# Kernel tuning notes

Hardware: AMD Instinct MI355X
Metric: run time of the kernel (lower is better)

## Reference

```python
import jax, jax.numpy as jnp
import numpy as np

B, C, H, W = 8, 256, 64, 64
K = 64  # tfam_channels

def _conv3x3(x, w, b):
    # x: [B,C,H,W], w: [O,I,3,3]
    y = jax.lax.conv_general_dilated(x, w, window_strides=(1, 1), padding='SAME',
                                     dimension_numbers=('NCHW', 'OIHW', 'NCHW'))
    return y + b[None, :, None, None]

def setup_inputs() -> dict:
    key = jax.random.key(0)
    ks = jax.random.split(key, 5)
    s1 = 1.0 / np.sqrt(C)
    s3 = 1.0 / np.sqrt(C * 9)
    return {
        'x': jax.random.normal(ks[0], (B, C, H, W), jnp.float32),
        'top_w': jax.random.normal(ks[1], (K, C), jnp.float32) * s1,
        'top_b': jnp.zeros((K,), jnp.float32),
        'center_w': jax.random.normal(ks[2], (K, C), jnp.float32) * s1,
        'center_b': jnp.zeros((K,), jnp.float32),
        'bottom_w': jax.random.normal(ks[3], (C, C, 3, 3), jnp.float32) * s3,
        'bottom_b': jnp.zeros((C,), jnp.float32),
        'out_w': jax.random.normal(ks[4], (C, C, 3, 3), jnp.float32) * s3,
        'out_b': jnp.zeros((C,), jnp.float32),
    }

def reference(x, top_w, top_b, center_w, center_b, bottom_w, bottom_b, out_w, out_b):
    b, c, h, w = x.shape
    hw = h * w
    # 1x1 convs as channel contractions
    x_top = jnp.einsum('bchw,kc->bkhw', x, top_w) + top_b[None, :, None, None]
    x_center = jnp.einsum('bchw,kc->bkhw', x, center_w) + center_b[None, :, None, None]
    x_bottom = _conv3x3(x, bottom_w, bottom_b)

    x_top = x_top.reshape(b, -1, hw)                     # [B,K,HW]
    x_center = x_center.reshape(b, -1, hw)               # [B,K,HW]
    x_bot = x_bottom.reshape(b, c, hw).transpose(0, 2, 1)  # [B,HW,C]

    sp_map = jnp.einsum('bkn,bkm->bnm', x_center, x_top)  # [B,HW,HW]
    # global softmax over the entire flattened map per batch element
    sp_map = jax.nn.softmax(sp_map.reshape(b, -1), axis=1).reshape(b, hw, hw)
    sp_map = jnp.einsum('bnm,bmc->bnc', sp_map, x_bot)    # [B,HW,C]
    # faithful raw reshape (as in the torch code: no transpose)
    sp_map = sp_map.reshape(b, c, h, w)
    y = x + sp_map
    return _conv3x3(y, out_w, out_b)
```

## Files before the change

### kernel.cpp

```cpp
#include <hip/hip_runtime.h>

using bf16x8 = __attribute__((ext_vector_type(8))) short;
using f16x8  = __attribute__((ext_vector_type(8))) _Float16;
using f32x4  = __attribute__((ext_vector_type(4))) float;

#define DEVI static __device__ __forceinline__

DEVI unsigned short f2bf(float f){
  unsigned u = __builtin_bit_cast(unsigned, f);
  u += 0x7fffu + ((u >> 16) & 1u);
  return (unsigned short)(u >> 16);
}
DEVI unsigned short f2h(float f){
  _Float16 h = (_Float16)f;
  return __builtin_bit_cast(unsigned short, h);
}
DEVI f32x4 zf4(){ f32x4 z; z[0]=0.f; z[1]=0.f; z[2]=0.f; z[3]=0.f; return z; }

__global__ __launch_bounds__(256) void k_prep(
    const float* __restrict__ top_w, const float* __restrict__ cen_w,
    const float* __restrict__ bot_w, const float* __restrict__ out_w,
    float* __restrict__ wTt, float* __restrict__ wTc,
    unsigned short* __restrict__ apb, unsigned short* __restrict__ apo){
  int i = blockIdx.x * 256 + threadIdx.x;
  if (i < 64 * 256){
    int c = i >> 6, k = i & 63;
    wTt[i] = top_w[k * 256 + c];
    wTc[i] = cen_w[k * 256 + c];
  }
  if (i < 9 * 256 * 256){
    int tau = i >> 16, oc = i & 65535;
    apb[i] = f2bf(bot_w[oc * 9 + tau]);
    apo[i] = f2bf(out_w[oc * 9 + tau]);
  }
}

__global__ __launch_bounds__(256) void k_topcenter(
    const float* __restrict__ x,
    const float* __restrict__ wTt, const float* __restrict__ wTc,
    const float* __restrict__ top_b, const float* __restrict__ cen_b,
    unsigned short* __restrict__ tT16, unsigned short* __restrict__ cT16){
  __shared__ float xs[16][256];
  int b = blockIdx.z, z = blockIdx.y, nt = blockIdx.x;
  int t = threadIdx.x;
  int n = nt * 256 + t;
  const float* wT   = z ? wTc : wTt;
  const float* bias = z ? cen_b : top_b;
  unsigned short* o16 = z ? cT16 : tT16;
  const float scale = z ? 1.0f : 1.4426950408889634f;
  const float* xb = x + ((size_t)b << 20);

  float acc[64];
  #pragma unroll
  for (int k = 0; k < 64; k++) acc[k] = 0.f;

  for (int cc = 0; cc < 256; cc += 16){
    __syncthreads();
    #pragma unroll
    for (int r = 0; r < 16; r++)
      xs[r][t] = xb[((size_t)(cc + r) << 12) + nt * 256 + t];
    __syncthreads();
    #pragma unroll
    for (int r = 0; r < 16; r++){
      float xv = xs[r][t];
      const float* wr = wT + (cc + r) * 64;
      #pragma unroll
      for (int k = 0; k < 64; k++) acc[k] = fmaf(wr[k], xv, acc[k]);
    }
  }
  size_t base = (((size_t)b << 12) + n) * 64;
  #pragma unroll
  for (int k8 = 0; k8 < 64; k8 += 8){
    bf16x8 v8;
    #pragma unroll
    for (int j = 0; j < 8; j++)
      v8[j] = (short)f2h((acc[k8 + j] + bias[k8 + j]) * scale);
    *(bf16x8*)(o16 + base + k8) = v8;
  }
}

__global__ __launch_bounds__(256) void k_trans(
    const float* __restrict__ x, const float* __restrict__ U0,
    const float* __restrict__ U1, const float* __restrict__ Z,
    unsigned short* __restrict__ ocl){
  __shared__ float tile[32][33];
  int b = blockIdx.z, ct = blockIdx.y, pt = blockIdx.x;
  int tx = threadIdx.x & 31, ty = threadIdx.x >> 5;
  size_t bo = (size_t)b << 20;
  int c0 = ct * 32, p0 = pt * 32;
  float invZ = (U0 != nullptr) ? (1.0f / Z[b]) : 0.0f;
  #pragma unroll
  for (int q = 0; q < 4; q++){
    int c = c0 + ty + q * 8;
    size_t idx = bo + ((size_t)c << 12) + p0 + tx;
    float v = x[idx];
    if (U0){
      float u = U0[idx];
      if (U1) u += U1[idx];
      v = fmaf(u, invZ, v);
    }
    tile[ty + q * 8][tx] = v;
  }
  __syncthreads();
  #pragma unroll
  for (int q = 0; q < 4; q++){
    int p = p0 + ty + q * 8;
    ocl[bo + ((size_t)p << 8) + c0 + tx] = f2bf(tile[tx][ty + q * 8]);
  }
}

template<int OUTF32>
__global__ __launch_bounds__(256, 4) void k_conv3(
    const unsigned short* __restrict__ incl,
    const unsigned short* __restrict__ ap,
    const float* __restrict__ bias, void* __restrict__ outp){
  __shared__ unsigned short Xs[3][64][72];
  int bid = blockIdx.x;
  int b = bid & 7, h = (bid >> 3) & 63, oh = bid >> 9;
  int t = threadIdx.x, wv = t >> 6, l = t & 63, lr = l & 15, g = l >> 4;
  int o0 = oh * 128 + wv * 32;
  const unsigned short* inb = incl + ((size_t)b << 20);

  f32x4 acc[2][4];
  #pragma unroll
  for (int a = 0; a < 2; a++)
    #pragma unroll
    for (int c = 0; c < 4; c++) acc[a][c] = zf4();

  int sw = t >> 2, sco = (t & 3) * 16;
  const bf16x8 zero8 = {0,0,0,0,0,0,0,0};

  bf16x8 st[3][2];
  #pragma unroll
  for (int r = 0; r < 3; r++){
    int h2 = h + r - 1;
    bool v = (unsigned)h2 < 64u;
    #pragma unroll
    for (int u = 0; u < 2; u++)
      st[r][u] = v ? *(const bf16x8*)(inb + (((size_t)(h2 * 64 + sw)) << 8)
                                      + sco + u * 8)
                   : zero8;
  }

  for (int cc = 0; cc < 256; cc += 64){
    __syncthreads();
    #pragma unroll
    for (int r = 0; r < 3; r++)
      #pragma unroll
      for (int u = 0; u < 2; u++)
        *(bf16x8*)(&Xs[r][sw][sco + u * 8]) = st[r][u];
    __syncthreads();
    if (cc < 192){
      #pragma unroll
      for (int r = 0; r < 3; r++){
        int h2 = h + r - 1;
        bool v = (unsigned)h2 < 64u;
        #pragma unroll
        for (int u = 0; u < 2; u++)
          st[r][u] = v ? *(const bf16x8*)(inb + (((size_t)(h2 * 64 + sw)) << 8)
                                          + cc + 64 + sco + u * 8)
                       : zero8;
      }
    }
    #pragma unroll
    for (int tau = 0; tau < 9; tau++){
      int dy = tau / 3 - 1, dx = tau % 3 - 1;
      #pragma unroll
      for (int kf = 0; kf < 2; kf++){
        bf16x8 af[2];
        #pragma unroll
        for (int of = 0; of < 2; of++)
          af[of] = *(const bf16x8*)(ap + ((size_t)tau << 16)
                     + ((o0 + of * 16 + lr) << 8) + cc + kf * 32 + 8 * g);
        bf16x8 bv[4];
        #pragma unroll
        for (int pf = 0; pf < 4; pf++){
          int wsrc = pf * 16 + lr + dx;
          bv[pf] = ((unsigned)wsrc < 64u)
                 ? *(const bf16x8*)(&Xs[dy + 1][wsrc][kf * 32 + 8 * g])
                 : zero8;
        }
        #pragma unroll
        for (int of = 0; of < 2; of++)
          #pragma unroll
          for (int pf = 0; pf < 4; pf++)
            acc[of][pf] = __builtin_amdgcn_mfma_f32_16x16x32_bf16(af[of], bv[pf], acc[of][pf], 0, 0, 0);
      }
    }
  }
  #pragma unroll
  for (int of = 0; of < 2; of++){
    int ob = o0 + of * 16 + 4 * g;
    #pragma unroll
    for (int pf = 0; pf < 4; pf++){
      int p = h * 64 + pf * 16 + lr;
      #pragma unroll
      for (int i = 0; i < 4; i++){
        int o = ob + i;
        float v = acc[of][pf][i] + bias[o];
        size_t oi = ((size_t)b << 20) + ((size_t)o << 12) + p;
        if (OUTF32) ((float*)outp)[oi] = v;
        else        ((unsigned short*)outp)[oi] = f2bf(v);
      }
    }
  }
}

__global__ __launch_bounds__(256, 2) void k_pv(
    const unsigned short* __restrict__ tT16, const unsigned short* __restrict__ cT16,
    const unsigned short* __restrict__ xbot,
    float* __restrict__ U0, float* __restrict__ U1,
    float* __restrict__ rsum, int nsteps){
  __shared__ unsigned short Pl[2][64 * 64];
  __shared__ unsigned short Xl[2][256 * 64];
  int bid = blockIdx.x;
  int b = bid & 7, nt = (bid >> 3) & 63, mh = bid >> 9;
  int t = threadIdx.x, wv = t >> 6, l = t & 63, lr = l & 15, g = l >> 4;
  int n0 = nt * 64;
  const unsigned short* xbb = xbot + ((size_t)b << 20);
  float* Ub = mh ? U1 : U0;

  f16x8 ch[2][4];
  #pragma unroll
  for (int kf = 0; kf < 2; kf++)
    #pragma unroll
    for (int nf = 0; nf < 4; nf++)
      ch[kf][nf] = *(const f16x8*)(cT16
          + (((size_t)b << 12) + n0 + nf * 16 + lr) * 64 + kf * 32 + 8 * g);

  f32x4 acc[4][4];
  #pragma unroll
  for (int a = 0; a < 4; a++)
    #pragma unroll
    for (int c = 0; c < 4; c++) acc[a][c] = zf4();
  float racc = 0.f;
  unsigned pk[4][2];

  int srow = wv * 8 + (l >> 3);
  const unsigned short* gstage = xbb + ((size_t)srow << 12) + (size_t)mh * 2048
      + (((l & 7) ^ ((l >> 3) & 7)) << 3);

  const unsigned short* tb = tT16
      + (((size_t)b << 12) + (size_t)mh * 2048 + wv * 16 + lr) * 64 + 8 * g;

  auto gll = [&](int buf, int step){
    const unsigned short* gs = gstage + (size_t)step * 64;
    #pragma unroll
    for (int j = 0; j < 8; j++)
      __builtin_amdgcn_global_load_lds(
          (const __attribute__((address_space(1))) void*)(gs + ((size_t)(32 * j) << 12)),
          (__attribute__((address_space(3))) void*)(&Xl[buf][(wv * 8 + j * 32) * 64]),
          16, 0, 0);
  };

  auto sphase = [&](f16x8 A0, f16x8 A1){
    f32x4 sa[4];
    #pragma unroll
    for (int nf = 0; nf < 4; nf++) sa[nf] = zf4();
    #pragma unroll
    for (int nf = 0; nf < 4; nf++)
      sa[nf] = __builtin_amdgcn_mfma_f32_16x16x32_f16(A0, ch[0][nf], sa[nf], 0, 0, 0);
    #pragma unroll
    for (int nf = 0; nf < 4; nf++)
      sa[nf] = __builtin_amdgcn_mfma_f32_16x16x32_f16(A1, ch[1][nf], sa[nf], 0, 0, 0);
    #pragma unroll
    for (int nf = 0; nf < 4; nf++){
      float e0 = __builtin_amdgcn_exp2f(sa[nf][0]);
      float e1 = __builtin_amdgcn_exp2f(sa[nf][1]);
      float e2 = __builtin_amdgcn_exp2f(sa[nf][2]);
      float e3 = __builtin_amdgcn_exp2f(sa[nf][3]);
      racc += (e0 + e1) + (e2 + e3);
      pk[nf][0] = (unsigned)f2bf(e0) | ((unsigned)f2bf(e1) << 16);
      pk[nf][1] = (unsigned)f2bf(e2) | ((unsigned)f2bf(e3) << 16);
    }
  };

  auto plwrite = [&](int buf){
    #pragma unroll
    for (int nf = 0; nf < 4; nf++){
      unsigned* pp = (unsigned*)(&Pl[buf][(nf * 16 + lr) * 64
          + (((2 * wv + (g >> 1)) ^ (lr & 7)) << 3) + ((g & 1) << 2)]);
      pp[0] = pk[nf][0];
      pp[1] = pk[nf][1];
    }
  };

  auto pv = [&](int buf){
    #pragma unroll
    for (int kf = 0; kf < 2; kf++){
      bf16x8 pa[4];
      #pragma unroll
      for (int nf = 0; nf < 4; nf++)
        pa[nf] = *(const bf16x8*)(&Pl[buf][(nf * 16 + lr) * 64
                   + ((((kf << 2) + g) ^ (lr & 7)) << 3)]);
      #pragma unroll
      for (int cf = 0; cf < 4; cf++){
        bf16x8 bx = *(const bf16x8*)(&Xl[buf][(wv * 64 + cf * 16 + lr) * 64
                   + ((((kf << 2) + g) ^ (lr & 7)) << 3)]);
        #pragma unroll
        for (int nf = 0; nf < 4; nf++)
          acc[nf][cf] = __builtin_amdgcn_mfma_f32_16x16x32_bf16(pa[nf], bx, acc[nf][cf], 0, 0, 0);
      }
    }
  };

  f16x8 a0 = *(const f16x8*)(tb);
  f16x8 a1 = *(const f16x8*)(tb + 32);
  gll(0, 0);
  sphase(a0, a1);
  a0 = *(const f16x8*)(tb + (size_t)4096);
  a1 = *(const f16x8*)(tb + (size_t)4096 + 32);
  plwrite(0);
  __syncthreads();

  for (int ms = 0; ms < nsteps; ms++){
    int cur = ms & 1, nxt = cur ^ 1;
    if (ms + 1 < nsteps){
      gll(nxt, ms + 1);
      sphase(a0, a1);
      if (ms + 2 < nsteps){
        a0 = *(const f16x8*)(tb + (size_t)(ms + 2) * 4096);
        a1 = *(const f16x8*)(tb + (size_t)(ms + 2) * 4096 + 32);
      }
    }
    pv(cur);
    if (ms + 1 < nsteps) plwrite(nxt);
    __syncthreads();
  }

  #pragma unroll
  for (int nf = 0; nf < 4; nf++)
    #pragma unroll
    for (int cf = 0; cf < 4; cf++)
      #pragma unroll
      for (int i = 0; i < 4; i++){
        int n = n0 + nf * 16 + 4 * g + i;
        int c = wv * 64 + cf * 16 + lr;
        __builtin_nontemporal_store(acc[nf][cf][i],
            &Ub[((size_t)b << 20) + ((size_t)n << 8) + c]);
      }
  racc += __shfl_xor(racc, 1);
  racc += __shfl_xor(racc, 2);
  racc += __shfl_xor(racc, 4);
  racc += __shfl_xor(racc, 8);
  racc += __shfl_xor(racc, 16);
  racc += __shfl_xor(racc, 32);
  if (l == 0) rsum[(size_t)bid * 4 + wv] = racc;
}

__global__ __launch_bounds__(256) void k_rsum(const float* __restrict__ r,
                                              float* __restrict__ Z, int msplit){
  __shared__ float red[256];
  int b = blockIdx.x, t = threadIdx.x;
  int total = 256 * msplit;
  float s = 0.f;
  for (int s2 = t; s2 < total; s2 += 256)
    s += r[(size_t)(b + 8 * (s2 >> 2)) * 4 + (s2 & 3)];
  red[t] = s;
  __syncthreads();
  for (int o = 128; o > 0; o >>= 1){
    if (t < o) red[t] += red[t + o];
    __syncthreads();
  }
  if (t == 0) Z[b] = red[0];
}

extern "C" void kernel_launch(void* const* d_in, const int* in_sizes, int n_in,
                              void* d_out, int out_size, void* d_ws, size_t ws_size,
                              hipStream_t stream) {
  const float* x     = (const float*)d_in[0];
  const float* top_w = (const float*)d_in[1];
  const float* top_b = (const float*)d_in[2];
  const float* cen_w = (const float*)d_in[3];
  const float* cen_b = (const float*)d_in[4];
  const float* bot_w = (const float*)d_in[5];
  const float* bot_b = (const float*)d_in[6];
  const float* out_w = (const float*)d_in[7];
  const float* out_b = (const float*)d_in[8];
  float* out = (float*)d_out;

  constexpr size_t MB = 1ull << 20;
  int msplit = (ws_size >= 108 * MB) ? 2 : 1;

  char* p = (char*)d_ws;
  float* U0 = (float*)p;                       p += 32 * MB;
  float* U1 = nullptr;
  if (msplit == 2){ U1 = (float*)p;            p += 32 * MB; }
  unsigned short* tT16 = (unsigned short*)p;   p += 4 * MB;
  unsigned short* cT16 = (unsigned short*)p;   p += 4 * MB;
  unsigned short* xbot = (unsigned short*)p;   p += 16 * MB;
  unsigned short* xcl  = (unsigned short*)p;   p += 16 * MB;
  float* wTt = (float*)p;                      p += 65536;
  float* wTc = (float*)p;                      p += 65536;
  unsigned short* apb = (unsigned short*)p;    p += 1179648;
  unsigned short* apo = (unsigned short*)p;    p += 1179648;
  float* r = (float*)p;                        p += 65536;
  float* Z = (float*)p;

  k_prep<<<2304, 256, 0, stream>>>(top_w, cen_w, bot_w, out_w, wTt, wTc, apb, apo);
  k_topcenter<<<dim3(16, 2, 8), 256, 0, stream>>>(x, wTt, wTc, top_b, cen_b,
                                                  tT16, cT16);
  k_trans<<<dim3(128, 8, 8), 256, 0, stream>>>(x, nullptr, nullptr, nullptr, xcl);
  k_conv3<0><<<dim3(1024), 256, 0, stream>>>(xcl, apb, bot_b, (void*)xbot);
  k_pv<<<dim3(512 * msplit), 256, 0, stream>>>(tT16, cT16, xbot, U0,
                                               msplit == 2 ? U1 : U0, r,
                                               64 / msplit);
  k_rsum<<<8, 256, 0, stream>>>(r, Z, msplit);
  k_trans<<<dim3(128, 8, 8), 256, 0, stream>>>(x, U0, U1, Z, xcl);
  k_conv3<1><<<dim3(1024), 256, 0, stream>>>(xcl, apo, out_b, (void*)out);
}
```

Baseline: 377.9 us.

## Fuse input transpose into top/center conv, shrink PV tiles, store partials as bf16

Result: slower. 583.2 us (+54.3%).

```diff
diff --git a/kernel.cpp b/kernel.cpp
--- a/kernel.cpp
+++ b/kernel.cpp
@@ -10,6 +10,10 @@
   unsigned u = __builtin_bit_cast(unsigned, f);
   u += 0x7fffu + ((u >> 16) & 1u);
   return (unsigned short)(u >> 16);
+}
+DEVI float bf2f(unsigned short h){
+  unsigned u = ((unsigned)h) << 16;
+  return __builtin_bit_cast(float, u);
 }
 DEVI unsigned short f2h(float f){
   _Float16 h = (_Float16)f;
@@ -39,7 +43,8 @@
     const float* __restrict__ x,
     const float* __restrict__ wTt, const float* __restrict__ wTc,
     const float* __restrict__ top_b, const float* __restrict__ cen_b,
-    unsigned short* __restrict__ tT16, unsigned short* __restrict__ cT16){
+    unsigned short* __restrict__ tT16, unsigned short* __restrict__ cT16,
+    unsigned short* __restrict__ xcl){
   __shared__ float xs[16][256];
   int b = blockIdx.z, z = blockIdx.y, nt = blockIdx.x;
   int t = threadIdx.x;
@@ -48,7 +53,8 @@
   const float* bias = z ? cen_b : top_b;
   unsigned short* o16 = z ? cT16 : tT16;
   const float scale = z ? 1.0f : 1.4426950408889634f;
-  const float* xb = x + ((size_t)b << 20);
+  size_t bo = (size_t)b << 20;
+  const float* xb = x + bo;
 
   float acc[64];
   #pragma unroll
@@ -67,8 +73,19 @@
       #pragma unroll
       for (int k = 0; k < 64; k++) acc[k] = fmaf(wr[k], xv, acc[k]);
     }
-  }
-  size_t base = (((size_t)b << 12) + n) * 64;
+    if (z == 0){
+      bf16x8 w0, w1;
+      #pragma unroll
+      for (int r = 0; r < 8; r++){
+        w0[r] = (short)f2bf(xs[r][t]);
+        w1[r] = (short)f2bf(xs[r + 8][t]);
+      }
+      *(bf16x8*)(xcl + bo + ((size_t)n << 8) + cc)     = w0;
+      *(bf16x8*)(xcl + bo + ((size_t)n << 8) + cc + 8) = w1;
+    }
+  }
+  size_t base = (bo >> 20 << 20 >> 8 << 8, (((size_t)b << 12) + n) * 64);
+  base = (((size_t)b << 12) + n) * 64;
   #pragma unroll
   for (int k8 = 0; k8 < 64; k8 += 8){
     bf16x8 v8;
@@ -80,26 +97,22 @@
 }
 
 __global__ __launch_bounds__(256) void k_trans(
-    const float* __restrict__ x, const float* __restrict__ U0,
-    const float* __restrict__ U1, const float* __restrict__ Z,
+    const float* __restrict__ x, const unsigned short* __restrict__ U0,
+    const unsigned short* __restrict__ U1, const float* __restrict__ Z,
     unsigned short* __restrict__ ocl){
   __shared__ float tile[32][33];
   int b = blockIdx.z, ct = blockIdx.y, pt = blockIdx.x;
   int tx = threadIdx.x & 31, ty = threadIdx.x >> 5;
   size_t bo = (size_t)b << 20;
   int c0 = ct * 32, p0 = pt * 32;
-  float invZ = (U0 != nullptr) ? (1.0f / Z[b]) : 0.0f;
+  float invZ = 1.0f / Z[b];
   #pragma unroll
   for (int q = 0; q < 4; q++){
     int c = c0 + ty + q * 8;
     size_t idx = bo + ((size_t)c << 12) + p0 + tx;
-    float v = x[idx];
-    if (U0){
-      float u = U0[idx];
-      if (U1) u += U1[idx];
-      v = fmaf(u, invZ, v);
-    }
-    tile[ty + q * 8][tx] = v;
+    float u = bf2f(U0[idx]);
+    if (U1) u += bf2f(U1[idx]);
+    tile[ty + q * 8][tx] = fmaf(u, invZ, x[idx]);
   }
   __syncthreads();
   #pragma unroll
@@ -206,27 +219,28 @@
   }
 }
 
-__global__ __launch_bounds__(256, 2) void k_pv(
+__global__ __launch_bounds__(256, 4) void k_pv(
     const unsigned short* __restrict__ tT16, const unsigned short* __restrict__ cT16,
     const unsigned short* __restrict__ xbot,
-    float* __restrict__ U0, float* __restrict__ U1,
+    unsigned short* __restrict__ U0, unsigned short* __restrict__ U1,
     float* __restrict__ rsum, int nsteps){
-  __shared__ unsigned short Pl[2][64 * 64];
-  __shared__ unsigned short Xl[2][256 * 64];
+  __shared__ unsigned short Pl[2][64 * 32];
+  __shared__ unsigned short Xl[2][256 * 32];
   int bid = blockIdx.x;
   int b = bid & 7, nt = (bid >> 3) & 63, mh = bid >> 9;
   int t = threadIdx.x, wv = t >> 6, l = t & 63, lr = l & 15, g = l >> 4;
   int n0 = nt * 64;
   const unsigned short* xbb = xbot + ((size_t)b << 20);
-  float* Ub = mh ? U1 : U0;
-
-  f16x8 ch[2][4];
+  unsigned short* Ub = mh ? U1 : U0;
+
+  f16x8 ch[2][2];
   #pragma unroll
   for (int kf = 0; kf < 2; kf++)
     #pragma unroll
-    for (int nf = 0; nf < 4; nf++)
+    for (int nf = 0; nf < 2; nf++)
       ch[kf][nf] = *(const f16x8*)(cT16
-          + (((size_t)b << 12) + n0 + nf * 16 + lr) * 64 + kf * 32 + 8 * g);
+          + (((size_t)b << 12) + n0 + (wv >> 1) * 32 + nf * 16 + lr) * 64
+          + kf * 32 + 8 * g);
 
   f32x4 acc[4][4];
   #pragma unroll
@@ -234,37 +248,38 @@
     #pragma unroll
     for (int c = 0; c < 4; c++) acc[a][c] = zf4();
   float racc = 0.f;
-  unsigned pk[4][2];
-
-  int srow = wv * 8 + (l >> 3);
-  const unsigned short* gstage = xbb + ((size_t)srow << 12) + (size_t)mh * 2048
-      + (((l & 7) ^ ((l >> 3) & 7)) << 3);
+  unsigned pk[2][2];
 
   const unsigned short* tb = tT16
-      + (((size_t)b << 12) + (size_t)mh * 2048 + wv * 16 + lr) * 64 + 8 * g;
+      + (((size_t)b << 12) + (size_t)mh * 2048 + (wv & 1) * 16 + lr) * 64 + 8 * g;
+
+  int rl = l >> 2;
+  int swzl = (rl & 3) ^ (rl >> 2);
+  const unsigned short* gstage = xbb
+      + ((size_t)(wv * 64 + rl) << 12) + (size_t)mh * 2048
+      + (((l & 3) ^ swzl) << 3);
 
   auto gll = [&](int buf, int step){
-    const unsigned short* gs = gstage + (size_t)step * 64;
-    #pragma unroll
-    for (int j = 0; j < 8; j++)
+    const unsigned short* gs = gstage + (size_t)step * 32;
+    #pragma unroll
+    for (int j = 0; j < 4; j++)
       __builtin_amdgcn_global_load_lds(
-          (const __attribute__((address_space(1))) void*)(gs + ((size_t)(32 * j) << 12)),
-          (__attribute__((address_space(3))) void*)(&Xl[buf][(wv * 8 + j * 32) * 64]),
+          (const __attribute__((address_space(1))) void*)(gs + ((size_t)(16 * j) << 12)),
+          (__attribute__((address_space(3))) void*)(&Xl[buf][(wv * 64 + j * 16) * 32]),
           16, 0, 0);
   };
 
   auto sphase = [&](f16x8 A0, f16x8 A1){
-    f32x4 sa[4];
-    #pragma unroll
-    for (int nf = 0; nf < 4; nf++) sa[nf] = zf4();
-    #pragma unroll
-    for (int nf = 0; nf < 4; nf++)
+    f32x4 sa[2];
+    sa[0] = zf4(); sa[1] = zf4();
+    #pragma unroll
+    for (int nf = 0; nf < 2; nf++)
       sa[nf] = __builtin_amdgcn_mfma_f32_16x16x32_f16(A0, ch[0][nf], sa[nf], 0, 0, 0);
     #pragma unroll
-    for (int nf = 0; nf < 4; nf++)
+    for (int nf = 0; nf < 2; nf++)
       sa[nf] = __builtin_amdgcn_mfma_f32_16x16x32_f16(A1, ch[1][nf], sa[nf], 0, 0, 0);
     #pragma unroll
-    for (int nf = 0; nf < 4; nf++){
+    for (int nf = 0; nf < 2; nf++){
       float e0 = __builtin_amdgcn_exp2f(sa[nf][0]);
       float e1 = __builtin_amdgcn_exp2f(sa[nf][1]);
       float e2 = __builtin_amdgcn_exp2f(sa[nf][2]);
@@ -275,32 +290,30 @@
     }
   };
 
+  int mt2 = (wv & 1) * 2 + (g >> 1);
   auto plwrite = [&](int buf){
     #pragma unroll
-    for (int nf = 0; nf < 4; nf++){
-      unsigned* pp = (unsigned*)(&Pl[buf][(nf * 16 + lr) * 64
-          + (((2 * wv + (g >> 1)) ^ (lr & 7)) << 3) + ((g & 1) << 2)]);
+    for (int nf = 0; nf < 2; nf++){
+      int n = (wv >> 1) * 32 + nf * 16 + lr;
+      int slot = mt2 ^ (lr & 3) ^ (lr >> 2);
+      unsigned* pp = (unsigned*)(&Pl[buf][n * 32 + slot * 8 + (g & 1) * 4]);
       pp[0] = pk[nf][0];
       pp[1] = pk[nf][1];
     }
   };
 
+  int rswz = (g ^ (lr & 3) ^ (lr >> 2)) * 8;
   auto pv = [&](int buf){
-    #pragma unroll
-    for (int kf = 0; kf < 2; kf++){
-      bf16x8 pa[4];
+    bf16x8 pa[4];
+    #pragma unroll
+    for (int nf = 0; nf < 4; nf++)
+      pa[nf] = *(const bf16x8*)(&Pl[buf][(nf * 16 + lr) * 32 + rswz]);
+    #pragma unroll
+    for (int cf = 0; cf < 4; cf++){
+      bf16x8 bx = *(const bf16x8*)(&Xl[buf][(wv * 64 + cf * 16 + lr) * 32 + rswz]);
       #pragma unroll
       for (int nf = 0; nf < 4; nf++)
-        pa[nf] = *(const bf16x8*)(&Pl[buf][(nf * 16 + lr) * 64
-                   + ((((kf << 2) + g) ^ (lr & 7)) << 3)]);
-      #pragma unroll
-      for (int cf = 0; cf < 4; cf++){
-        bf16x8 bx = *(const bf16x8*)(&Xl[buf][(wv * 64 + cf * 16 + lr) * 64
-                   + ((((kf << 2) + g) ^ (lr & 7)) << 3)]);
-        #pragma unroll
-        for (int nf = 0; nf < 4; nf++)
-          acc[nf][cf] = __builtin_amdgcn_mfma_f32_16x16x32_bf16(pa[nf], bx, acc[nf][cf], 0, 0, 0);
-      }
+        acc[nf][cf] = __builtin_amdgcn_mfma_f32_16x16x32_bf16(pa[nf], bx, acc[nf][cf], 0, 0, 0);
     }
   };
 
@@ -308,8 +321,8 @@
   f16x8 a1 = *(const f16x8*)(tb + 32);
   gll(0, 0);
   sphase(a0, a1);
-  a0 = *(const f16x8*)(tb + (size_t)4096);
-  a1 = *(const f16x8*)(tb + (size_t)4096 + 32);
+  a0 = *(const f16x8*)(tb + 2048);
+  a1 = *(const f16x8*)(tb + 2048 + 32);
   plwrite(0);
   __syncthreads();
 
@@ -319,8 +332,8 @@
       gll(nxt, ms + 1);
       sphase(a0, a1);
       if (ms + 2 < nsteps){
-        a0 = *(const f16x8*)(tb + (size_t)(ms + 2) * 4096);
-        a1 = *(const f16x8*)(tb + (size_t)(ms + 2) * 4096 + 32);
+        a0 = *(const f16x8*)(tb + (size_t)(ms + 2) * 2048);
+        a1 = *(const f16x8*)(tb + (size_t)(ms + 2) * 2048 + 32);
       }
     }
     pv(cur);
@@ -336,7 +349,7 @@
       for (int i = 0; i < 4; i++){
         int n = n0 + nf * 16 + 4 * g + i;
         int c = wv * 64 + cf * 16 + lr;
-        __builtin_nontemporal_store(acc[nf][cf][i],
+        __builtin_nontemporal_store(f2bf(acc[nf][cf][i]),
             &Ub[((size_t)b << 20) + ((size_t)n << 8) + c]);
       }
   racc += __shfl_xor(racc, 1);
@@ -380,12 +393,12 @@
   float* out = (float*)d_out;
 
   constexpr size_t MB = 1ull << 20;
-  int msplit = (ws_size >= 108 * MB) ? 2 : 1;
+  int msplit = (ws_size >= 80 * MB) ? 2 : 1;
 
   char* p = (char*)d_ws;
-  float* U0 = (float*)p;                       p += 32 * MB;
-  float* U1 = nullptr;
-  if (msplit == 2){ U1 = (float*)p;            p += 32 * MB; }
+  unsigned short* U0 = (unsigned short*)p;     p += 16 * MB;
+  unsigned short* U1 = nullptr;
+  if (msplit == 2){ U1 = (unsigned short*)p;   p += 16 * MB; }
   unsigned short* tT16 = (unsigned short*)p;   p += 4 * MB;
   unsigned short* cT16 = (unsigned short*)p;   p += 4 * MB;
   unsigned short* xbot = (unsigned short*)p;   p += 16 * MB;
@@ -399,12 +412,11 @@
 
   k_prep<<<2304, 256, 0, stream>>>(top_w, cen_w, bot_w, out_w, wTt, wTc, apb, apo);
   k_topcenter<<<dim3(16, 2, 8), 256, 0, stream>>>(x, wTt, wTc, top_b, cen_b,
-                                                  tT16, cT16);
-  k_trans<<<dim3(128, 8, 8), 256, 0, stream>>>(x, nullptr, nullptr, nullptr, xcl);
+                                                  tT16, cT16, xcl);
   k_conv3<0><<<dim3(1024), 256, 0, stream>>>(xcl, apb, bot_b, (void*)xbot);
   k_pv<<<dim3(512 * msplit), 256, 0, stream>>>(tT16, cT16, xbot, U0,
                                                msplit == 2 ? U1 : U0, r,
-                                               64 / msplit);
+                                               2048 / (32 * msplit) * 2);
   k_rsum<<<8, 256, 0, stream>>>(r, Z, msplit);
   k_trans<<<dim3(128, 8, 8), 256, 0, stream>>>(x, U0, U1, Z, xcl);
   k_conv3<1><<<dim3(1024), 256, 0, stream>>>(xcl, apo, out_b, (void*)out);
```
